# Optimization experiments

Measured on AMD Instinct MI355X. Metric: run time of the kernel, lower is better.

## Reference

```python
import jax, jax.numpy as jnp
import numpy as np

NUM_NODES = 100000
EMBED_DIM = 128
HIDDEN_DIM = 512
NUM_EDGES = 2000000      # E: number of (node, hyperedge) incidences
NUM_HYPEREDGES = 100000  # H: static stand-in for edge_idx.max()+1
LN_EPS = 1e-5


def setup_inputs() -> dict:
    key = jax.random.key(0)
    k_ne, k_ni, k_ei, k_w1, k_b1, k_w2, k_b2 = jax.random.split(key, 7)
    node_embeds = jax.random.normal(k_ne, (NUM_NODES, EMBED_DIM), dtype=jnp.float32)
    node_idx = jax.random.randint(k_ni, (NUM_EDGES,), 0, NUM_NODES)
    # guarantee every hyperedge id in [0, H) appears so max()+1 == NUM_HYPEREDGES
    edge_idx = jnp.concatenate([
        jnp.arange(NUM_HYPEREDGES),
        jax.random.randint(k_ei, (NUM_EDGES - NUM_HYPEREDGES,), 0, NUM_HYPEREDGES),
    ])
    hyperedge_index = jnp.stack([node_idx, edge_idx]).astype(jnp.int32)
    s1 = 1.0 / np.sqrt(2 * EMBED_DIM)
    s2 = 1.0 / np.sqrt(HIDDEN_DIM)
    return {
        "node_embeds": node_embeds,
        "hyperedge_index": hyperedge_index,
        "W1": jax.random.uniform(k_w1, (2 * EMBED_DIM, HIDDEN_DIM), jnp.float32, -s1, s1),
        "b1": jax.random.uniform(k_b1, (HIDDEN_DIM,), jnp.float32, -s1, s1),
        "gamma": jnp.ones((HIDDEN_DIM,), jnp.float32),
        "beta": jnp.zeros((HIDDEN_DIM,), jnp.float32),
        "W2": jax.random.uniform(k_w2, (HIDDEN_DIM, 1), jnp.float32, -s2, s2),
        "b2": jax.random.uniform(k_b2, (1,), jnp.float32, -s2, s2),
    }


def reference(node_embeds, hyperedge_index, W1, b1, gamma, beta, W2, b2):
    node_idx, edge_idx = hyperedge_index[0], hyperedge_index[1]
    gathered = node_embeds[node_idx]  # [E, d] irregular gather
    # scatter-mean
    seg_sum = jax.ops.segment_sum(gathered, edge_idx, num_segments=NUM_HYPEREDGES)  # [H, d]
    counts = jax.ops.segment_sum(jnp.ones((gathered.shape[0],), gathered.dtype), edge_idx,
                                 num_segments=NUM_HYPEREDGES)  # [H]
    nonempty = counts > 0
    mean_pooled = seg_sum / jnp.maximum(counts, 1.0)[:, None]
    # scatter-max (empty segments -> 0, matching torch_scatter fill)
    seg_max = jax.ops.segment_max(gathered, edge_idx, num_segments=NUM_HYPEREDGES)
    max_pooled = jnp.where(nonempty[:, None], seg_max, 0.0)
    h = jnp.concatenate([mean_pooled, max_pooled], axis=1)  # [H, 2d]
    # MLP: Linear -> LayerNorm -> ReLU -> Linear
    z = h @ W1 + b1
    mu = jnp.mean(z, axis=-1, keepdims=True)
    var = jnp.mean(jnp.square(z - mu), axis=-1, keepdims=True)
    z = (z - mu) * jax.lax.rsqrt(var + LN_EPS) * gamma + beta
    z = jax.nn.relu(z)
    return (z @ W2 + b2).squeeze(-1)  # [H]
```

## Files before the change

kernel.cpp:

```cpp
#include <hip/hip_runtime.h>
#include <hip/hip_bf16.h>

#define NUM_NODES 100000
#define EMBED_DIM 128
#define HIDDEN_DIM 512
#define NUM_EDGES 2000000
#define NUM_H 100000
#define LN_EPS 1e-5f
#define NCHUNK 98

#define OFF_COUNTS   0
#define OFF_CURSOR   100096
#define OFF_OFFSETS  200192
#define OFF_SORTED   300288
#define OFF_PARTIALS 2300288
#define OFF_BASES    2300416
#define OFF_W1HI     2300544
#define OFF_W1LO     2366080

typedef __attribute__((ext_vector_type(8))) short bf16x8;
typedef __attribute__((ext_vector_type(4))) float f32x4;

__device__ __forceinline__ unsigned short f2bf(float x) {
    unsigned u = __float_as_uint(x);
    u += 0x7fff + ((u >> 16) & 1);
    return (unsigned short)(u >> 16);
}
__device__ __forceinline__ float bf2f(unsigned short h) {
    return __uint_as_float(((unsigned)h) << 16);
}

__global__ __launch_bounds__(256) void pack_w1(const float* __restrict__ W1,
                                               unsigned short* __restrict__ hi,
                                               unsigned short* __restrict__ lo) {
    int e = blockIdx.x * 256 + threadIdx.x;
    int t = e >> 14, rem = e & 16383;
    int n = rem >> 5, gj = rem & 31;
    int k = t * 32 + gj;
    float x = W1[k * HIDDEN_DIM + n];
    unsigned short h = f2bf(x);
    hi[e] = h;
    lo[e] = f2bf(x - bf2f(h));
}

__global__ __launch_bounds__(256) void hist_kernel(const int* __restrict__ eidx,
                                                   int* __restrict__ counts) {
    int e = blockIdx.x * 256 + threadIdx.x;
    if (e < NUM_EDGES) atomicAdd(&counts[eidx[e]], 1);
}

__global__ __launch_bounds__(1024) void scan_partial(const int* __restrict__ counts,
                                                     int* __restrict__ offsets,
                                                     int* __restrict__ partials) {
    __shared__ int wsum[16];
    __shared__ int woff[16];
    const int tid = threadIdx.x, b = blockIdx.x;
    const int warp = tid >> 6, lane = tid & 63;
    const int i = b * 1024 + tid;
    int v = (i < NUM_H) ? counts[i] : 0;
    int incl = v;
    #pragma unroll
    for (int off = 1; off < 64; off <<= 1) {
        int t = __shfl(incl, lane - off);
        if (lane >= off) incl += t;
    }
    if (lane == 63) wsum[warp] = incl;
    __syncthreads();
    if (tid < 16) {
        int s = wsum[tid], is = s;
        #pragma unroll
        for (int off = 1; off < 16; off <<= 1) {
            int t = __shfl(is, tid - off);
            if (tid >= off) is += t;
        }
        woff[tid] = is - s;
    }
    __syncthreads();
    if (i < NUM_H) offsets[i] = woff[warp] + incl - v;
    if (tid == 0) partials[b] = woff[15] + wsum[15];
}

__global__ __launch_bounds__(128) void scan_base(const int* __restrict__ partials,
                                                 int* __restrict__ bases) {
    __shared__ int t0;
    const int tid = threadIdx.x;
    const int lane = tid & 63, w = tid >> 6;
    int v = (tid < NCHUNK) ? partials[tid] : 0;
    int incl = v;
    #pragma unroll
    for (int off = 1; off < 64; off <<= 1) {
        int t = __shfl(incl, lane - off);
        if (lane >= off) incl += t;
    }
    if (tid == 63) t0 = incl;
    __syncthreads();
    bases[tid] = incl - v + (w ? t0 : 0);
}

__global__ __launch_bounds__(1024) void scan_add(int* __restrict__ offsets,
                                                 const int* __restrict__ bases) {
    const int i = blockIdx.x * 1024 + threadIdx.x;
    if (i < NUM_H) offsets[i] += bases[blockIdx.x];
    if (i == 0) offsets[NUM_H] = NUM_EDGES;
}

__global__ __launch_bounds__(256) void scatter_kernel(const int* __restrict__ nidx,
                                                      const int* __restrict__ eidx,
                                                      const int* __restrict__ offsets,
                                                      int* __restrict__ cursor,
                                                      int* __restrict__ sorted) {
    int e = blockIdx.x * 256 + threadIdx.x;
    if (e < NUM_EDGES) {
        int h = eidx[e];
        int pos = offsets[h] + atomicAdd(&cursor[h], 1);
        sorted[pos] = nidx[e];
    }
}

__global__ __launch_bounds__(256) void fused_mlp_kernel(
        const float* __restrict__ embeds,
        const int* __restrict__ offsets,
        const int* __restrict__ sorted,
        const char* __restrict__ w1pack,
        const float* __restrict__ b1,
        const float* __restrict__ gamma, const float* __restrict__ beta,
        const float* __restrict__ W2, const float* __restrict__ b2,
        float* __restrict__ out) {
    __shared__ __align__(16) char A_hi[8192];
    __shared__ __align__(16) char A_lo[8192];
    __shared__ float red_s[4][16];
    __shared__ float red_q[4][16];
    __shared__ float red_d[4][16];

    const int tid  = threadIdx.x;
    const int warp = tid >> 6;
    const int lane = tid & 63;
    const int m0   = blockIdx.x * 16;

    for (int rr = 0; rr < 4; ++rr) {
        const int row = warp * 4 + rr;
        const int hh  = m0 + row;
        const int beg = offsets[hh], end = offsets[hh + 1];
        float2 s0 = {0.f, 0.f}, s1 = {0.f, 0.f}, s2 = {0.f, 0.f}, s3 = {0.f, 0.f};
        float2 x0 = {-3.4e38f, -3.4e38f}, x1 = x0, x2 = x0, x3 = x0;
        int i = beg;
        for (; i + 4 <= end; i += 4) {
            int n0 = sorted[i], n1 = sorted[i + 1], n2 = sorted[i + 2], n3 = sorted[i + 3];
            float2 v0 = *(const float2*)&embeds[(size_t)n0 * EMBED_DIM + lane * 2];
            float2 v1 = *(const float2*)&embeds[(size_t)n1 * EMBED_DIM + lane * 2];
            float2 v2 = *(const float2*)&embeds[(size_t)n2 * EMBED_DIM + lane * 2];
            float2 v3 = *(const float2*)&embeds[(size_t)n3 * EMBED_DIM + lane * 2];
            s0.x += v0.x; s0.y += v0.y; x0.x = fmaxf(x0.x, v0.x); x0.y = fmaxf(x0.y, v0.y);
            s1.x += v1.x; s1.y += v1.y; x1.x = fmaxf(x1.x, v1.x); x1.y = fmaxf(x1.y, v1.y);
            s2.x += v2.x; s2.y += v2.y; x2.x = fmaxf(x2.x, v2.x); x2.y = fmaxf(x2.y, v2.y);
            s3.x += v3.x; s3.y += v3.y; x3.x = fmaxf(x3.x, v3.x); x3.y = fmaxf(x3.y, v3.y);
        }
        for (; i < end; ++i) {
            int n0 = sorted[i];
            float2 v0 = *(const float2*)&embeds[(size_t)n0 * EMBED_DIM + lane * 2];
            s0.x += v0.x; s0.y += v0.y; x0.x = fmaxf(x0.x, v0.x); x0.y = fmaxf(x0.y, v0.y);
        }
        const int deg = end - beg;
        const float inv = deg ? 1.f / (float)deg : 0.f;
        float2 mean = {(s0.x + s1.x + s2.x + s3.x) * inv, (s0.y + s1.y + s2.y + s3.y) * inv};
        float2 mx   = {fmaxf(fmaxf(x0.x, x1.x), fmaxf(x2.x, x3.x)),
                       fmaxf(fmaxf(x0.y, x1.y), fmaxf(x2.y, x3.y))};
        if (!deg) { mx.x = 0.f; mx.y = 0.f; }
        const unsigned swz = ((unsigned)(row & 7)) << 4;
        const unsigned bm  = ((unsigned)(row * 512 + lane * 4)) ^ swz;
        const unsigned bx  = ((unsigned)(row * 512 + 256 + lane * 4)) ^ swz;
        unsigned short h0 = f2bf(mean.x), h1 = f2bf(mean.y);
        *(unsigned*)(A_hi + bm) = (unsigned)h0 | ((unsigned)h1 << 16);
        *(unsigned*)(A_lo + bm) = (unsigned)f2bf(mean.x - bf2f(h0)) |
                                  ((unsigned)f2bf(mean.y - bf2f(h1)) << 16);
        unsigned short g0 = f2bf(mx.x), g1 = f2bf(mx.y);
        *(unsigned*)(A_hi + bx) = (unsigned)g0 | ((unsigned)g1 << 16);
        *(unsigned*)(A_lo + bx) = (unsigned)f2bf(mx.x - bf2f(g0)) |
                                  ((unsigned)f2bf(mx.y - bf2f(g1)) << 16);
    }
    __syncthreads();

    const int c = lane & 15, g = lane >> 4;
    const int wbase = warp * 128;
    f32x4 acc[8];
    #pragma unroll
    for (int nt = 0; nt < 8; ++nt) acc[nt] = (f32x4){0.f, 0.f, 0.f, 0.f};

    const char* bptr = w1pack + (size_t)((wbase + c) * 64 + g * 16);
    const unsigned swzA = ((unsigned)(c & 7)) << 4;
    #pragma unroll
    for (int t = 0; t < 8; ++t) {
        const unsigned ab = ((unsigned)(c * 512 + t * 64 + g * 16)) ^ swzA;
        bf16x8 ahi = *(const bf16x8*)(A_hi + ab);
        bf16x8 alo = *(const bf16x8*)(A_lo + ab);
        #pragma unroll
        for (int nt = 0; nt < 8; ++nt) {
            const char* p = bptr + t * 32768 + nt * 1024;
            bf16x8 bhi = *(const bf16x8*)p;
            bf16x8 blo = *(const bf16x8*)(p + 262144);
            acc[nt] = __builtin_amdgcn_mfma_f32_16x16x32_bf16(ahi, bhi, acc[nt], 0, 0, 0);
            acc[nt] = __builtin_amdgcn_mfma_f32_16x16x32_bf16(alo, bhi, acc[nt], 0, 0, 0);
            acc[nt] = __builtin_amdgcn_mfma_f32_16x16x32_bf16(ahi, blo, acc[nt], 0, 0, 0);
        }
    }

    float b1v[8], gv[8], bev[8], w2v[8];
    #pragma unroll
    for (int nt = 0; nt < 8; ++nt) {
        const int col = wbase + nt * 16 + c;
        b1v[nt] = b1[col]; gv[nt] = gamma[col]; bev[nt] = beta[col]; w2v[nt] = W2[col];
    }
    float zv[8][4];
    float s[4], sq[4];
    #pragma unroll
    for (int q = 0; q < 4; ++q) { s[q] = 0.f; sq[q] = 0.f; }
    #pragma unroll
    for (int nt = 0; nt < 8; ++nt)
        #pragma unroll
        for (int q = 0; q < 4; ++q) {
            float z = acc[nt][q] + b1v[nt];
            zv[nt][q] = z;
            s[q] += z; sq[q] += z * z;
        }
    #pragma unroll
    for (int q = 0; q < 4; ++q)
        #pragma unroll
        for (int off = 1; off < 16; off <<= 1) {
            s[q]  += __shfl_xor(s[q],  off);
            sq[q] += __shfl_xor(sq[q], off);
        }
    if (c == 0)
        #pragma unroll
        for (int q = 0; q < 4; ++q) {
            red_s[warp][g * 4 + q] = s[q];
            red_q[warp][g * 4 + q] = sq[q];
        }
    __syncthreads();
    float d[4];
    #pragma unroll
    for (int q = 0; q < 4; ++q) {
        const int row = g * 4 + q;
        float S = red_s[0][row] + red_s[1][row] + red_s[2][row] + red_s[3][row];
        float Q = red_q[0][row] + red_q[1][row] + red_q[2][row] + red_q[3][row];
        float mu = S * (1.f / 512.f);
        float var = Q * (1.f / 512.f) - mu * mu;
        float rs = rsqrtf(var + LN_EPS);
        float acc_d = 0.f;
        #pragma unroll
        for (int nt = 0; nt < 8; ++nt) {
            float y = (zv[nt][q] - mu) * rs * gv[nt] + bev[nt];
            y = fmaxf(y, 0.f);
            acc_d += y * w2v[nt];
        }
        d[q] = acc_d;
    }
    #pragma unroll
    for (int q = 0; q < 4; ++q)
        #pragma unroll
        for (int off = 1; off < 16; off <<= 1) d[q] += __shfl_xor(d[q], off);
    if (c == 0)
        #pragma unroll
        for (int q = 0; q < 4; ++q) red_d[warp][g * 4 + q] = d[q];
    __syncthreads();
    if (tid < 16)
        out[m0 + tid] = red_d[0][tid] + red_d[1][tid] + red_d[2][tid] + red_d[3][tid] + b2[0];
}

extern "C" void kernel_launch(void* const* d_in, const int* in_sizes, int n_in,
                              void* d_out, int out_size, void* d_ws, size_t ws_size,
                              hipStream_t stream) {
    const float* embeds = (const float*)d_in[0];
    const int*   hidx   = (const int*)d_in[1];
    const float* W1     = (const float*)d_in[2];
    const float* b1     = (const float*)d_in[3];
    const float* gamma  = (const float*)d_in[4];
    const float* beta   = (const float*)d_in[5];
    const float* W2     = (const float*)d_in[6];
    const float* b2     = (const float*)d_in[7];
    float*       out    = (float*)d_out;

    int* ws       = (int*)d_ws;
    int* counts   = ws + OFF_COUNTS;
    int* cursor   = ws + OFF_CURSOR;
    int* offsets  = ws + OFF_OFFSETS;
    int* sorted   = ws + OFF_SORTED;
    int* partials = ws + OFF_PARTIALS;
    int* bases    = ws + OFF_BASES;
    unsigned short* w1hi = (unsigned short*)(ws + OFF_W1HI);
    unsigned short* w1lo = (unsigned short*)(ws + OFF_W1LO);

    const int* nidx = hidx;
    const int* eidx = hidx + NUM_EDGES;

    hipMemsetAsync(d_ws, 0, (size_t)OFF_OFFSETS * sizeof(int), stream);

    pack_w1<<<512, 256, 0, stream>>>(W1, w1hi, w1lo);
    const int eb = (NUM_EDGES + 255) / 256;
    hist_kernel<<<eb, 256, 0, stream>>>(eidx, counts);
    scan_partial<<<NCHUNK, 1024, 0, stream>>>(counts, offsets, partials);
    scan_base<<<1, 128, 0, stream>>>(partials, bases);
    scan_add<<<NCHUNK, 1024, 0, stream>>>(offsets, bases);
    scatter_kernel<<<eb, 256, 0, stream>>>(nidx, eidx, offsets, cursor, sorted);
    fused_mlp_kernel<<<NUM_H / 16, 256, 0, stream>>>(embeds, offsets, sorted,
                                                     (const char*)(ws + OFF_W1HI),
                                                     b1, gamma, beta, W2, b2, out);
}
```

Measured before the change: 613.4 us.

## Balance segment reduction across warps with LDS atomics and 32-row MLP tiles

The fused kernel now handles 32 hyperedges per block. Instead of one warp owning each row, all warps stride over the block's whole contiguous edge range. They accumulate sums with LDS float atomics and maxima with order-preserving unsigned atomicMax, using a row tag packed into the high bits of the sorted node index. The MFMA stage processes two 16-row tiles per weight load, halving W1 global reads per row. Histogram and scatter kernels read indices as int4, four edges per thread. The cost is LDS atomic contention and float-sum reordering in exchange for better load balance across variable-degree rows.

```diff
diff --git a/kernel.cpp b/kernel.cpp
--- a/kernel.cpp
+++ b/kernel.cpp
@@ -28,6 +28,14 @@
 }
 __device__ __forceinline__ float bf2f(unsigned short h) {
     return __uint_as_float(((unsigned)h) << 16);
+}
+__device__ __forceinline__ unsigned fmap(float f) {
+    int i = __float_as_int(f);
+    return (i >= 0) ? (((unsigned)i) | 0x80000000u) : ~((unsigned)i);
+}
+__device__ __forceinline__ float funmap(unsigned u) {
+    unsigned i = (u & 0x80000000u) ? (u & 0x7FFFFFFFu) : ~u;
+    return __int_as_float((int)i);
 }
 
 __global__ __launch_bounds__(256) void pack_w1(const float* __restrict__ W1,
@@ -43,10 +51,16 @@
     lo[e] = f2bf(x - bf2f(h));
 }
 
-__global__ __launch_bounds__(256) void hist_kernel(const int* __restrict__ eidx,
+__global__ __launch_bounds__(256) void hist_kernel(const int4* __restrict__ eidx4,
                                                    int* __restrict__ counts) {
     int e = blockIdx.x * 256 + threadIdx.x;
-    if (e < NUM_EDGES) atomicAdd(&counts[eidx[e]], 1);
+    if (e < NUM_EDGES / 4) {
+        int4 v = eidx4[e];
+        atomicAdd(&counts[v.x], 1);
+        atomicAdd(&counts[v.y], 1);
+        atomicAdd(&counts[v.z], 1);
+        atomicAdd(&counts[v.w], 1);
+    }
 }
 
 __global__ __launch_bounds__(1024) void scan_partial(const int* __restrict__ counts,
@@ -104,16 +118,31 @@
     if (i == 0) offsets[NUM_H] = NUM_EDGES;
 }
 
-__global__ __launch_bounds__(256) void scatter_kernel(const int* __restrict__ nidx,
-                                                      const int* __restrict__ eidx,
+__global__ __launch_bounds__(256) void scatter_kernel(const int4* __restrict__ nidx4,
+                                                      const int4* __restrict__ eidx4,
                                                       const int* __restrict__ offsets,
                                                       int* __restrict__ cursor,
                                                       int* __restrict__ sorted) {
     int e = blockIdx.x * 256 + threadIdx.x;
-    if (e < NUM_EDGES) {
-        int h = eidx[e];
-        int pos = offsets[h] + atomicAdd(&cursor[h], 1);
-        sorted[pos] = nidx[e];
+    if (e < NUM_EDGES / 4) {
+        int4 n = nidx4[e];
+        int4 h = eidx4[e];
+        {
+            int pos = offsets[h.x] + atomicAdd(&cursor[h.x], 1);
+            sorted[pos] = n.x | ((h.x & 31) << 20);
+        }
+        {
+            int pos = offsets[h.y] + atomicAdd(&cursor[h.y], 1);
+            sorted[pos] = n.y | ((h.y & 31) << 20);
+        }
+        {
+            int pos = offsets[h.z] + atomicAdd(&cursor[h.z], 1);
+            sorted[pos] = n.z | ((h.z & 31) << 20);
+        }
+        {
+            int pos = offsets[h.w] + atomicAdd(&cursor[h.w], 1);
+            sorted[pos] = n.w | ((h.w & 31) << 20);
+        }
     }
 }
 
@@ -126,81 +155,119 @@
         const float* __restrict__ gamma, const float* __restrict__ beta,
         const float* __restrict__ W2, const float* __restrict__ b2,
         float* __restrict__ out) {
-    __shared__ __align__(16) char A_hi[8192];
-    __shared__ __align__(16) char A_lo[8192];
-    __shared__ float red_s[4][16];
-    __shared__ float red_q[4][16];
-    __shared__ float red_d[4][16];
+    __shared__ __align__(16) float accum[8192];
+    __shared__ float red_s[4][32];
+    __shared__ float red_q[4][32];
+    __shared__ float red_d[4][32];
+    __shared__ int sOff[33];
 
     const int tid  = threadIdx.x;
     const int warp = tid >> 6;
     const int lane = tid & 63;
-    const int m0   = blockIdx.x * 16;
-
-    for (int rr = 0; rr < 4; ++rr) {
-        const int row = warp * 4 + rr;
-        const int hh  = m0 + row;
-        const int beg = offsets[hh], end = offsets[hh + 1];
-        float2 s0 = {0.f, 0.f}, s1 = {0.f, 0.f}, s2 = {0.f, 0.f}, s3 = {0.f, 0.f};
-        float2 x0 = {-3.4e38f, -3.4e38f}, x1 = x0, x2 = x0, x3 = x0;
-        int i = beg;
-        for (; i + 4 <= end; i += 4) {
-            int n0 = sorted[i], n1 = sorted[i + 1], n2 = sorted[i + 2], n3 = sorted[i + 3];
-            float2 v0 = *(const float2*)&embeds[(size_t)n0 * EMBED_DIM + lane * 2];
-            float2 v1 = *(const float2*)&embeds[(size_t)n1 * EMBED_DIM + lane * 2];
-            float2 v2 = *(const float2*)&embeds[(size_t)n2 * EMBED_DIM + lane * 2];
-            float2 v3 = *(const float2*)&embeds[(size_t)n3 * EMBED_DIM + lane * 2];
-            s0.x += v0.x; s0.y += v0.y; x0.x = fmaxf(x0.x, v0.x); x0.y = fmaxf(x0.y, v0.y);
-            s1.x += v1.x; s1.y += v1.y; x1.x = fmaxf(x1.x, v1.x); x1.y = fmaxf(x1.y, v1.y);
-            s2.x += v2.x; s2.y += v2.y; x2.x = fmaxf(x2.x, v2.x); x2.y = fmaxf(x2.y, v2.y);
-            s3.x += v3.x; s3.y += v3.y; x3.x = fmaxf(x3.x, v3.x); x3.y = fmaxf(x3.y, v3.y);
-        }
-        for (; i < end; ++i) {
-            int n0 = sorted[i];
-            float2 v0 = *(const float2*)&embeds[(size_t)n0 * EMBED_DIM + lane * 2];
-            s0.x += v0.x; s0.y += v0.y; x0.x = fmaxf(x0.x, v0.x); x0.y = fmaxf(x0.y, v0.y);
-        }
-        const int deg = end - beg;
+    const int m0   = blockIdx.x * 32;
+
+    #pragma unroll
+    for (int i = 0; i < 8; ++i)
+        ((f32x4*)accum)[tid + 256 * i] = (f32x4){0.f, 0.f, 0.f, 0.f};
+    if (tid < 33) sOff[tid] = offsets[m0 + tid];
+    __syncthreads();
+
+    float*    sumb = accum;
+    unsigned* maxb = (unsigned*)accum + 4096;
+
+    const int segBeg = sOff[0], segEnd = sOff[32];
+    int p0 = segBeg + warp * 8;
+    int cur[8];
+    #pragma unroll
+    for (int k = 0; k < 8; ++k) cur[k] = (p0 + k < segEnd) ? sorted[p0 + k] : -1;
+    while (p0 < segEnd) {
+        const int p1 = p0 + 32;
+        int nxt[8];
+        #pragma unroll
+        for (int k = 0; k < 8; ++k) nxt[k] = (p1 + k < segEnd) ? sorted[p1 + k] : -1;
+        float va[8], vb[8];
+        #pragma unroll
+        for (int k = 0; k < 8; ++k) {
+            if (cur[k] >= 0) {
+                const int node = cur[k] & 0xFFFFF;
+                va[k] = embeds[node * EMBED_DIM + lane];
+                vb[k] = embeds[node * EMBED_DIM + 64 + lane];
+            }
+        }
+        #pragma unroll
+        for (int k = 0; k < 8; ++k) {
+            if (cur[k] >= 0) {
+                const int row = cur[k] >> 20;
+                atomicAdd(&sumb[row * 128 + lane], va[k]);
+                atomicAdd(&sumb[row * 128 + 64 + lane], vb[k]);
+                atomicMax(&maxb[row * 128 + lane], fmap(va[k]));
+                atomicMax(&maxb[row * 128 + 64 + lane], fmap(vb[k]));
+            }
+        }
+        #pragma unroll
+        for (int k = 0; k < 8; ++k) cur[k] = nxt[k];
+        p0 = p1;
+    }
+    __syncthreads();
+
+    float mA[8], mB[8], xA[8], xB[8];
+    #pragma unroll
+    for (int rr = 0; rr < 8; ++rr) {
+        const int row = warp * 8 + rr;
+        const int deg = sOff[row + 1] - sOff[row];
         const float inv = deg ? 1.f / (float)deg : 0.f;
-        float2 mean = {(s0.x + s1.x + s2.x + s3.x) * inv, (s0.y + s1.y + s2.y + s3.y) * inv};
-        float2 mx   = {fmaxf(fmaxf(x0.x, x1.x), fmaxf(x2.x, x3.x)),
-                       fmaxf(fmaxf(x0.y, x1.y), fmaxf(x2.y, x3.y))};
-        if (!deg) { mx.x = 0.f; mx.y = 0.f; }
+        mA[rr] = sumb[row * 128 + lane] * inv;
+        mB[rr] = sumb[row * 128 + 64 + lane] * inv;
+        xA[rr] = deg ? funmap(maxb[row * 128 + lane]) : 0.f;
+        xB[rr] = deg ? funmap(maxb[row * 128 + 64 + lane]) : 0.f;
+    }
+    __syncthreads();
+
+    char* Ab = (char*)accum;
+    #pragma unroll
+    for (int rr = 0; rr < 8; ++rr) {
+        const int row = warp * 8 + rr;
         const unsigned swz = ((unsigned)(row & 7)) << 4;
-        const unsigned bm  = ((unsigned)(row * 512 + lane * 4)) ^ swz;
-        const unsigned bx  = ((unsigned)(row * 512 + 256 + lane * 4)) ^ swz;
-        unsigned short h0 = f2bf(mean.x), h1 = f2bf(mean.y);
-        *(unsigned*)(A_hi + bm) = (unsigned)h0 | ((unsigned)h1 << 16);
-        *(unsigned*)(A_lo + bm) = (unsigned)f2bf(mean.x - bf2f(h0)) |
-                                  ((unsigned)f2bf(mean.y - bf2f(h1)) << 16);
-        unsigned short g0 = f2bf(mx.x), g1 = f2bf(mx.y);
-        *(unsigned*)(A_hi + bx) = (unsigned)g0 | ((unsigned)g1 << 16);
-        *(unsigned*)(A_lo + bx) = (unsigned)f2bf(mx.x - bf2f(g0)) |
-                                  ((unsigned)f2bf(mx.y - bf2f(g1)) << 16);
+        const float vals[4] = {mA[rr], mB[rr], xA[rr], xB[rr]};
+        const int   ks[4]   = {lane, lane + 64, 128 + lane, 192 + lane};
+        #pragma unroll
+        for (int j = 0; j < 4; ++j) {
+            const unsigned off = ((unsigned)(row * 512 + ks[j] * 2)) ^ swz;
+            const unsigned short hbits = f2bf(vals[j]);
+            *(unsigned short*)(Ab + off)         = hbits;
+            *(unsigned short*)(Ab + 16384 + off) = f2bf(vals[j] - bf2f(hbits));
+        }
     }
     __syncthreads();
 
     const int c = lane & 15, g = lane >> 4;
     const int wbase = warp * 128;
-    f32x4 acc[8];
-    #pragma unroll
-    for (int nt = 0; nt < 8; ++nt) acc[nt] = (f32x4){0.f, 0.f, 0.f, 0.f};
-
-    const char* bptr = w1pack + (size_t)((wbase + c) * 64 + g * 16);
+    f32x4 acc[2][8];
+    #pragma unroll
+    for (int rt = 0; rt < 2; ++rt)
+        #pragma unroll
+        for (int nt = 0; nt < 8; ++nt) acc[rt][nt] = (f32x4){0.f, 0.f, 0.f, 0.f};
+
+    const char* bp = w1pack + (size_t)((wbase + c) * 64 + g * 16);
     const unsigned swzA = ((unsigned)(c & 7)) << 4;
     #pragma unroll
     for (int t = 0; t < 8; ++t) {
-        const unsigned ab = ((unsigned)(c * 512 + t * 64 + g * 16)) ^ swzA;
-        bf16x8 ahi = *(const bf16x8*)(A_hi + ab);
-        bf16x8 alo = *(const bf16x8*)(A_lo + ab);
+        const unsigned a0 = ((unsigned)(c * 512 + t * 64 + g * 16)) ^ swzA;
+        bf16x8 ah0 = *(const bf16x8*)(Ab + a0);
+        bf16x8 al0 = *(const bf16x8*)(Ab + 16384 + a0);
+        bf16x8 ah1 = *(const bf16x8*)(Ab + 8192 + a0);
+        bf16x8 al1 = *(const bf16x8*)(Ab + 16384 + 8192 + a0);
         #pragma unroll
         for (int nt = 0; nt < 8; ++nt) {
-            const char* p = bptr + t * 32768 + nt * 1024;
-            bf16x8 bhi = *(const bf16x8*)p;
-            bf16x8 blo = *(const bf16x8*)(p + 262144);
-            acc[nt] = __builtin_amdgcn_mfma_f32_16x16x32_bf16(ahi, bhi, acc[nt], 0, 0, 0);
-            acc[nt] = __builtin_amdgcn_mfma_f32_16x16x32_bf16(alo, bhi, acc[nt], 0, 0, 0);
-            acc[nt] = __builtin_amdgcn_mfma_f32_16x16x32_bf16(ahi, blo, acc[nt], 0, 0, 0);
+            const char* p = bp + t * 32768 + nt * 1024;
+            bf16x8 bh = *(const bf16x8*)p;
+            bf16x8 bl = *(const bf16x8*)(p + 262144);
+            acc[0][nt] = __builtin_amdgcn_mfma_f32_16x16x32_bf16(ah0, bh, acc[0][nt], 0, 0, 0);
+            acc[0][nt] = __builtin_amdgcn_mfma_f32_16x16x32_bf16(al0, bh, acc[0][nt], 0, 0, 0);
+            acc[0][nt] = __builtin_amdgcn_mfma_f32_16x16x32_bf16(ah0, bl, acc[0][nt], 0, 0, 0);
+            acc[1][nt] = __builtin_amdgcn_mfma_f32_16x16x32_bf16(ah1, bh, acc[1][nt], 0, 0, 0);
+            acc[1][nt] = __builtin_amdgcn_mfma_f32_16x16x32_bf16(al1, bh, acc[1][nt], 0, 0, 0);
+            acc[1][nt] = __builtin_amdgcn_mfma_f32_16x16x32_bf16(ah1, bl, acc[1][nt], 0, 0, 0);
         }
     }
 
@@ -210,59 +277,72 @@
         const int col = wbase + nt * 16 + c;
         b1v[nt] = b1[col]; gv[nt] = gamma[col]; bev[nt] = beta[col]; w2v[nt] = W2[col];
     }
-    float zv[8][4];
-    float s[4], sq[4];
-    #pragma unroll
-    for (int q = 0; q < 4; ++q) { s[q] = 0.f; sq[q] = 0.f; }
-    #pragma unroll
-    for (int nt = 0; nt < 8; ++nt)
+    float s[2][4], sq[2][4];
+    #pragma unroll
+    for (int rt = 0; rt < 2; ++rt)
+        #pragma unroll
+        for (int q = 0; q < 4; ++q) { s[rt][q] = 0.f; sq[rt][q] = 0.f; }
+    #pragma unroll
+    for (int rt = 0; rt < 2; ++rt)
+        #pragma unroll
+        for (int nt = 0; nt < 8; ++nt)
+            #pragma unroll
+            for (int q = 0; q < 4; ++q) {
+                float z = acc[rt][nt][q] + b1v[nt];
+                acc[rt][nt][q] = z;
+                s[rt][q] += z; sq[rt][q] += z * z;
+            }
+    #pragma unroll
+    for (int rt = 0; rt < 2; ++rt)
+        #pragma unroll
+        for (int q = 0; q < 4; ++q)
+            #pragma unroll
+            for (int off = 1; off < 16; off <<= 1) {
+                s[rt][q]  += __shfl_xor(s[rt][q],  off);
+                sq[rt][q] += __shfl_xor(sq[rt][q], off);
+            }
+    if (c == 0)
+        #pragma unroll
+        for (int rt = 0; rt < 2; ++rt)
+            #pragma unroll
+            for (int q = 0; q < 4; ++q) {
+                red_s[warp][rt * 16 + g * 4 + q] = s[rt][q];
+                red_q[warp][rt * 16 + g * 4 + q] = sq[rt][q];
+            }
+    __syncthreads();
+    float d[2][4];
+    #pragma unroll
+    for (int rt = 0; rt < 2; ++rt)
         #pragma unroll
         for (int q = 0; q < 4; ++q) {
-            float z = acc[nt][q] + b1v[nt];
-            zv[nt][q] = z;
-            s[q] += z; sq[q] += z * z;
-        }
-    #pragma unroll
-    for (int q = 0; q < 4; ++q)
-        #pragma unroll
-        for (int off = 1; off < 16; off <<= 1) {
-            s[q]  += __shfl_xor(s[q],  off);
-            sq[q] += __shfl_xor(sq[q], off);
-        }
+            const int row = rt * 16 + g * 4 + q;
+            float S = red_s[0][row] + red_s[1][row] + red_s[2][row] + red_s[3][row];
+            float Q = red_q[0][row] + red_q[1][row] + red_q[2][row] + red_q[3][row];
+            float mu = S * (1.f / 512.f);
+            float var = Q * (1.f / 512.f) - mu * mu;
+            float rs = rsqrtf(var + LN_EPS);
+            float acc_d = 0.f;
+            #pragma unroll
+            for (int nt = 0; nt < 8; ++nt) {
+                float y = (acc[rt][nt][q] - mu) * rs * gv[nt] + bev[nt];
+                y = fmaxf(y, 0.f);
+                acc_d += y * w2v[nt];
+            }
+            d[rt][q] = acc_d;
+        }
+    #pragma unroll
+    for (int rt = 0; rt < 2; ++rt)
+        #pragma unroll
+        for (int q = 0; q < 4; ++q)
+            #pragma unroll
+            for (int off = 1; off < 16; off <<= 1) d[rt][q] += __shfl_xor(d[rt][q], off);
     if (c == 0)
         #pragma unroll
-        for (int q = 0; q < 4; ++q) {
-            red_s[warp][g * 4 + q] = s[q];
-            red_q[warp][g * 4 + q] = sq[q];
-        }
-    __syncthreads();
-    float d[4];
-    #pragma unroll
-    for (int q = 0; q < 4; ++q) {
-        const int row = g * 4 + q;
-        float S = red_s[0][row] + red_s[1][row] + red_s[2][row] + red_s[3][row];
-        float Q = red_q[0][row] + red_q[1][row] + red_q[2][row] + red_q[3][row];
-        float mu = S * (1.f / 512.f);
-        float var = Q * (1.f / 512.f) - mu * mu;
-        float rs = rsqrtf(var + LN_EPS);
-        float acc_d = 0.f;
-        #pragma unroll
-        for (int nt = 0; nt < 8; ++nt) {
-            float y = (zv[nt][q] - mu) * rs * gv[nt] + bev[nt];
-            y = fmaxf(y, 0.f);
-            acc_d += y * w2v[nt];
-        }
-        d[q] = acc_d;
-    }
-    #pragma unroll
-    for (int q = 0; q < 4; ++q)
-        #pragma unroll
-        for (int off = 1; off < 16; off <<= 1) d[q] += __shfl_xor(d[q], off);
-    if (c == 0)
-        #pragma unroll
-        for (int q = 0; q < 4; ++q) red_d[warp][g * 4 + q] = d[q];
-    __syncthreads();
-    if (tid < 16)
+        for (int rt = 0; rt < 2; ++rt)
+            #pragma unroll
+            for (int q = 0; q < 4; ++q) red_d[warp][rt * 16 + g * 4 + q] = d[rt][q];
+    __syncthreads();
+    if (tid < 32)
         out[m0 + tid] = red_d[0][tid] + red_d[1][tid] + red_d[2][tid] + red_d[3][tid] + b2[0];
 }
 
@@ -295,13 +375,14 @@
     hipMemsetAsync(d_ws, 0, (size_t)OFF_OFFSETS * sizeof(int), stream);
 
     pack_w1<<<512, 256, 0, stream>>>(W1, w1hi, w1lo);
-    const int eb = (NUM_EDGES + 255) / 256;
-    hist_kernel<<<eb, 256, 0, stream>>>(eidx, counts);
+    const int eb4 = (NUM_EDGES / 4 + 255) / 256;
+    hist_kernel<<<eb4, 256, 0, stream>>>((const int4*)eidx, counts);
     scan_partial<<<NCHUNK, 1024, 0, stream>>>(counts, offsets, partials);
     scan_base<<<1, 128, 0, stream>>>(partials, bases);
     scan_add<<<NCHUNK, 1024, 0, stream>>>(offsets, bases);
-    scatter_kernel<<<eb, 256, 0, stream>>>(nidx, eidx, offsets, cursor, sorted);
-    fused_mlp_kernel<<<NUM_H / 16, 256, 0, stream>>>(embeds, offsets, sorted,
+    scatter_kernel<<<eb4, 256, 0, stream>>>((const int4*)nidx, (const int4*)eidx,
+                                            offsets, cursor, sorted);
+    fused_mlp_kernel<<<NUM_H / 32, 256, 0, stream>>>(embeds, offsets, sorted,
                                                      (const char*)(ws + OFF_W1HI),
                                                      b1, gamma, beta, W2, b2, out);
 }
```

Measured after the change: 1.723 ms. +180.9%, slower.
